# Performance work log

Measured on AMD Instinct MI355X. Metric: run time of the kernel, lower is better.

The kernel has to match this reference:

```python
import jax, jax.numpy as jnp
import numpy as np

B, S, V, E, H = 2048, 128, 128, 300, 512  # batch, max_length, vocab, embed, hidden (enc_outstate_dim == H)


def setup_inputs() -> dict:
    key = jax.random.key(0)
    ks = jax.random.split(key, 20)
    s = 0.05
    return {
        "x": jax.random.randint(ks[0], (B, 1), 0, V),
        "hidden": jax.random.normal(ks[1], (1, B, H), jnp.float32),
        "enc_output": jax.random.normal(ks[2], (B, S, H), jnp.float32),
        "emb_table": jax.random.normal(ks[3], (V, E), jnp.float32) * s,
        "W1_w": jax.random.normal(ks[4], (H, H), jnp.float32) * s,
        "W1_b": jnp.zeros((H,), jnp.float32),
        "W2_w": jax.random.normal(ks[5], (H, H), jnp.float32) * s,
        "W2_b": jnp.zeros((H,), jnp.float32),
        "V_w": jax.random.normal(ks[6], (1, H), jnp.float32) * s,
        "V_b": jnp.zeros((1,), jnp.float32),
        "gru_w_ih": jax.random.normal(ks[7], (3 * H, E + H), jnp.float32) * s,
        "gru_w_hh": jax.random.normal(ks[8], (3 * H, H), jnp.float32) * s,
        "gru_b_ih": jnp.zeros((3 * H,), jnp.float32),
        "gru_b_hh": jnp.zeros((3 * H,), jnp.float32),
        "fc1_w": jax.random.normal(ks[9], (E, H), jnp.float32) * s,
        "fc1_b": jnp.zeros((E,), jnp.float32),
        "fc2_w": jax.random.normal(ks[10], (V, E), jnp.float32) * s,
        "fc2_b": jnp.zeros((V,), jnp.float32),
    }


def reference(x, hidden, enc_output, emb_table, W1_w, W1_b, W2_w, W2_b, V_w, V_b,
              gru_w_ih, gru_w_hh, gru_b_ih, gru_b_hh, fc1_w, fc1_b, fc2_w, fc2_b):
    emb = emb_table[x[:, 0]]  # [B,E]
    # Bahdanau additive attention
    hsum = jnp.sum(hidden, axis=0)  # [B,H] (sum over layers)
    score = jnp.tanh(enc_output @ W1_w.T + W1_b + (hsum @ W2_w.T + W2_b)[:, None, :])  # [B,S,H]
    attw = jax.nn.softmax(score @ V_w.T + V_b, axis=1)  # [B,S,1]
    ctx = jnp.sum(attw * enc_output, axis=1)  # [B,H]
    # single-step GRU (PyTorch gate layout: r,z,n)
    gin = jnp.concatenate([ctx, emb], axis=-1)  # [B,H+E]
    h0 = hidden[0]
    gi = gin @ gru_w_ih.T + gru_b_ih
    gh = h0 @ gru_w_hh.T + gru_b_hh
    i_r, i_z, i_n = gi[:, :H], gi[:, H:2 * H], gi[:, 2 * H:]
    h_r, h_z, h_n = gh[:, :H], gh[:, H:2 * H], gh[:, 2 * H:]
    r = jax.nn.sigmoid(i_r + h_r)
    z = jax.nn.sigmoid(i_z + h_z)
    n = jnp.tanh(i_n + r * h_n)
    h_new = (1.0 - z) * n + z * h0  # [B,H]
    # FC head
    y = jax.nn.leaky_relu(h_new @ fc1_w.T + fc1_b, 0.01) @ fc2_w.T + fc2_b  # [B,V]
    return y, h_new[None]
```

## Files before the change

kernel.cpp:

```cpp
#include <hip/hip_runtime.h>


typedef __attribute__((ext_vector_type(4))) float floatx4;
typedef __attribute__((ext_vector_type(8))) short short8;

#define DEV static __device__ __forceinline__

DEV unsigned short f2bf(float f) {
  unsigned u = __float_as_uint(f);
  u = u + 0x7fffu + ((u >> 16) & 1u);
  return (unsigned short)(u >> 16);
}
DEV float bf2f(unsigned short s) { return __uint_as_float(((unsigned)s) << 16); }
DEV float tanh_fast(float x) {
  float e = __expf(2.f * x);
  return 1.f - 2.f / (e + 1.f);
}
DEV float sigmoid_fast(float x) { return 1.f / (1.f + __expf(-x)); }

__global__ void convpad_kernel(const float* __restrict__ src,
                               unsigned short* __restrict__ dst,
                               int Nsrc, int Kin, int Kp) {
  int idx = blockIdx.x * 256 + threadIdx.x;
  int n = idx / Kp, k = idx - n * Kp;
  float v = (k < Kin && n < Nsrc) ? src[(size_t)n * Kin + k] : 0.f;
  dst[idx] = f2bf(v);
}

__global__ void prep_bias_kernel(const float* __restrict__ W1b,
                                 const float* __restrict__ W2b,
                                 float* __restrict__ keyb,
                                 const float* __restrict__ fc1b,
                                 float* __restrict__ fc1bp) {
  int i = blockIdx.x * 256 + threadIdx.x;
  if (i < 512) keyb[i] = W1b[i] + W2b[i];
  if (i < 384) fc1bp[i] = (i < 300) ? fc1b[i] : 0.f;
}

__global__ void emb_kernel(const int* __restrict__ x,
                           const float* __restrict__ embt,
                           unsigned short* __restrict__ gin) {
  int b = blockIdx.x, e = threadIdx.x;
  float v = (e < 300) ? embt[(size_t)x[b] * 300 + e] : 0.f;
  gin[(size_t)b * 832 + 512 + e] = f2bf(v);
}

template <int EPI>
__global__ __launch_bounds__(256, 3) void gemm_bt(
    const unsigned short* __restrict__ A, int lda,
    const unsigned short* __restrict__ Bm, int ldb,
    const float* __restrict__ bias,
    void* __restrict__ Cp, int ldc, int K) {
  __shared__ unsigned short As[128 * 64];
  __shared__ unsigned short Bs[128 * 64];
  int tid = threadIdx.x;
  int bm = blockIdx.x * 128, bn = blockIdx.y * 128;
  int lane = tid & 63, wave = tid >> 6;
  int l15 = lane & 15, l4 = lane >> 4;
  int wm = (wave >> 1) * 64, wn = (wave & 1) * 64;

  floatx4 zero = {0.f, 0.f, 0.f, 0.f};
  floatx4 acc[4][4];
#pragma unroll
  for (int i = 0; i < 4; ++i)
#pragma unroll
    for (int j = 0; j < 4; ++j) acc[i][j] = zero;

  int row = tid >> 1;
  int gc0 = (tid & 1) * 4;
  const unsigned short* Aptr = A + (size_t)(bm + row) * lda + gc0 * 8;
  const unsigned short* Bptr = Bm + (size_t)(bn + row) * ldb + gc0 * 8;
  int rslot7 = row & 7, lslot7 = l15 & 7;

  int nk = K >> 6;
  for (int kt = 0; kt < nk; ++kt) {
#pragma unroll
    for (int i = 0; i < 4; ++i) {
      int slot = (gc0 + i) ^ rslot7;
      *(uint4*)&As[row * 64 + slot * 8] = *(const uint4*)(Aptr + kt * 64 + i * 8);
      *(uint4*)&Bs[row * 64 + slot * 8] = *(const uint4*)(Bptr + kt * 64 + i * 8);
    }
    __syncthreads();
#pragma unroll
    for (int ks = 0; ks < 2; ++ks) {
      int slot = (ks * 4 + l4) ^ lslot7;
      short8 av[4], bv[4];
#pragma unroll
      for (int mt = 0; mt < 4; ++mt)
        av[mt] = *(const short8*)&As[(wm + mt * 16 + l15) * 64 + slot * 8];
#pragma unroll
      for (int nt = 0; nt < 4; ++nt)
        bv[nt] = *(const short8*)&Bs[(wn + nt * 16 + l15) * 64 + slot * 8];
#pragma unroll
      for (int mt = 0; mt < 4; ++mt)
#pragma unroll
        for (int nt = 0; nt < 4; ++nt)
          acc[mt][nt] = __builtin_amdgcn_mfma_f32_16x16x32_bf16(
              av[mt], bv[nt], acc[mt][nt], 0, 0, 0);
    }
    __syncthreads();
  }

#pragma unroll
  for (int nt = 0; nt < 4; ++nt) {
    int n = bn + wn + nt * 16 + l15;
    float bvv = bias[n];
#pragma unroll
    for (int mt = 0; mt < 4; ++mt) {
#pragma unroll
      for (int r = 0; r < 4; ++r) {
        int m = bm + wm + mt * 16 + l4 * 4 + r;
        float v = acc[mt][nt][r] + bvv;
        if (EPI == 1) {
          v = v > 0.f ? v : 0.01f * v;
          ((unsigned short*)Cp)[(size_t)m * ldc + n] = f2bf(v);
        } else {
          ((float*)Cp)[(size_t)m * ldc + n] = v;
        }
      }
    }
  }
}

#define ATTN_LDS_BYTES (128 * 512 * 2 + 2 * 128 * 4)

__global__ __launch_bounds__(512, 2) void attn_kernel(
    const float* __restrict__ enc, const unsigned short* __restrict__ W1b16,
    const float* __restrict__ key, const float* __restrict__ Vw,
    unsigned short* __restrict__ gin) {
  extern __shared__ unsigned char smem_raw[];
  unsigned short* Albs = (unsigned short*)smem_raw;
  float* lds_logits = (float*)(smem_raw + 128 * 512 * 2);
  float* lds_attw = lds_logits + 128;

  int b = blockIdx.x;
  int tid = threadIdx.x;
  const float* encb = enc + (size_t)b * 128 * 512;

  if (tid < 128) lds_logits[tid] = 0.f;

#pragma unroll 2
  for (int it = 0; it < 16; ++it) {
    int g = it * 512 + tid;
    int m = g >> 6, gc = g & 63;
    const float4* src = (const float4*)(encb + (size_t)g * 8);
    float4 lo = src[0], hi = src[1];
    uint4 pk;
    pk.x = (unsigned)f2bf(lo.x) | ((unsigned)f2bf(lo.y) << 16);
    pk.y = (unsigned)f2bf(lo.z) | ((unsigned)f2bf(lo.w) << 16);
    pk.z = (unsigned)f2bf(hi.x) | ((unsigned)f2bf(hi.y) << 16);
    pk.w = (unsigned)f2bf(hi.z) | ((unsigned)f2bf(hi.w) << 16);
    int slot = gc ^ (m & 7);
    *(uint4*)&Albs[m * 512 + slot * 8] = pk;
  }
  __syncthreads();

  int wave = tid >> 6, lane = tid & 63;
  int l15 = lane & 15, l4 = lane >> 4, lslot7 = l15 & 7;
  int n0 = wave * 64;

  floatx4 zero = {0.f, 0.f, 0.f, 0.f};
  floatx4 acc[8][4];
#pragma unroll
  for (int i = 0; i < 8; ++i)
#pragma unroll
    for (int j = 0; j < 4; ++j) acc[i][j] = zero;

#pragma unroll 2
  for (int kt = 0; kt < 16; ++kt) {
    int slot = (kt * 4 + l4) ^ lslot7;
    short8 av[8], bv[4];
#pragma unroll
    for (int nt = 0; nt < 4; ++nt) {
      int n = n0 + nt * 16 + l15;
      bv[nt] = *(const short8*)(W1b16 + (size_t)n * 512 + kt * 32 + l4 * 8);
    }
#pragma unroll
    for (int mt = 0; mt < 8; ++mt)
      av[mt] = *(const short8*)&Albs[(mt * 16 + l15) * 512 + slot * 8];
#pragma unroll
    for (int mt = 0; mt < 8; ++mt)
#pragma unroll
      for (int nt = 0; nt < 4; ++nt)
        acc[mt][nt] = __builtin_amdgcn_mfma_f32_16x16x32_bf16(
            av[mt], bv[nt], acc[mt][nt], 0, 0, 0);
  }

  float kb[4], vwl[4];
#pragma unroll
  for (int nt = 0; nt < 4; ++nt) {
    int col = n0 + nt * 16 + l15;
    kb[nt] = key[(size_t)b * 512 + col];
    vwl[nt] = Vw[col];
  }
#pragma unroll
  for (int mt = 0; mt < 8; ++mt) {
#pragma unroll
    for (int r = 0; r < 4; ++r) {
      float c = 0.f;
#pragma unroll
      for (int nt = 0; nt < 4; ++nt)
        c += tanh_fast(acc[mt][nt][r] + kb[nt]) * vwl[nt];
      c += __shfl_xor(c, 1, 64);
      c += __shfl_xor(c, 2, 64);
      c += __shfl_xor(c, 4, 64);
      c += __shfl_xor(c, 8, 64);
      if (l15 == 0) atomicAdd(&lds_logits[mt * 16 + l4 * 4 + r], c);
    }
  }
  __syncthreads();

  if (wave == 0) {
    float l0 = lds_logits[lane], l1 = lds_logits[lane + 64];
    float mx = fmaxf(l0, l1);
#pragma unroll
    for (int o = 32; o >= 1; o >>= 1) mx = fmaxf(mx, __shfl_xor(mx, o, 64));
    float e0 = __expf(l0 - mx), e1 = __expf(l1 - mx);
    float s = e0 + e1;
#pragma unroll
    for (int o = 32; o >= 1; o >>= 1) s += __shfl_xor(s, o, 64);
    float inv = 1.f / s;
    lds_attw[lane] = e0 * inv;
    lds_attw[lane + 64] = e1 * inv;
  }
  __syncthreads();

  int h = tid, gc = h >> 3, off = h & 7;
  float cx = 0.f;
  for (int s = 0; s < 128; ++s)
    cx += lds_attw[s] * bf2f(Albs[s * 512 + ((gc ^ (s & 7)) << 3) + off]);
  gin[(size_t)b * 832 + h] = f2bf(cx);
}

__global__ void gru_kernel(const float* __restrict__ gi,
                           const float* __restrict__ gh,
                           const float* __restrict__ hidden,
                           float* __restrict__ outh,
                           unsigned short* __restrict__ hnewbf) {
  int idx = blockIdx.x * 256 + threadIdx.x;
  int b = idx >> 9, h = idx & 511;
  const float* gib = gi + (size_t)b * 1536;
  const float* ghb = gh + (size_t)b * 1536;
  float r = sigmoid_fast(gib[h] + ghb[h]);
  float z = sigmoid_fast(gib[512 + h] + ghb[512 + h]);
  float n = tanh_fast(gib[1024 + h] + r * ghb[1024 + h]);
  float h0 = hidden[idx];
  float hn = (1.f - z) * n + z * h0;
  outh[idx] = hn;
  hnewbf[idx] = f2bf(hn);
}

extern "C" void kernel_launch(void* const* d_in, const int* in_sizes, int n_in,
                              void* d_out, int out_size, void* d_ws,
                              size_t ws_size, hipStream_t stream) {
  const int* x = (const int*)d_in[0];
  const float* hidden = (const float*)d_in[1];
  const float* enc = (const float*)d_in[2];
  const float* embt = (const float*)d_in[3];
  const float* W1w = (const float*)d_in[4];
  const float* W1b = (const float*)d_in[5];
  const float* W2w = (const float*)d_in[6];
  const float* W2b = (const float*)d_in[7];
  const float* Vw = (const float*)d_in[8];
  const float* wih = (const float*)d_in[10];
  const float* whh = (const float*)d_in[11];
  const float* bih = (const float*)d_in[12];
  const float* bhh = (const float*)d_in[13];
  const float* fc1w = (const float*)d_in[14];
  const float* fc1b = (const float*)d_in[15];
  const float* fc2w = (const float*)d_in[16];
  const float* fc2b = (const float*)d_in[17];

  float* out_y = (float*)d_out;
  float* out_h = out_y + 2048 * 128;

  char* ws = (char*)d_ws;
  size_t o = 0;
  auto alloc = [&](size_t bytes) {
    size_t r = o;
    o += (bytes + 255) & ~(size_t)255;
    return r;
  };
  unsigned short* W1bf = (unsigned short*)(ws + alloc(512 * 512 * 2));
  unsigned short* W2bf = (unsigned short*)(ws + alloc(512 * 512 * 2));
  unsigned short* wihbf = (unsigned short*)(ws + alloc(1536 * 832 * 2));
  unsigned short* whhbf = (unsigned short*)(ws + alloc(1536 * 512 * 2));
  unsigned short* fc1wbf = (unsigned short*)(ws + alloc(384 * 512 * 2));
  unsigned short* fc2wbf = (unsigned short*)(ws + alloc(128 * 384 * 2));
  unsigned short* hidbf = (unsigned short*)(ws + alloc(2048 * 512 * 2));
  unsigned short* ginbf = (unsigned short*)(ws + alloc((size_t)2048 * 832 * 2));
  float* keyb = (float*)(ws + alloc(512 * 4));
  float* fc1bp = (float*)(ws + alloc(384 * 4));
  float* key = (float*)(ws + alloc((size_t)2048 * 512 * 4));
  float* gi = (float*)(ws + alloc((size_t)2048 * 1536 * 4));
  float* gh = (float*)(ws + alloc((size_t)2048 * 1536 * 4));
  unsigned short* hnewbf = (unsigned short*)(ws + alloc(2048 * 512 * 2));
  unsigned short* a1bf = (unsigned short*)(ws + alloc((size_t)2048 * 384 * 2));

  convpad_kernel<<<512 * 512 / 256, 256, 0, stream>>>(W1w, W1bf, 512, 512, 512);
  convpad_kernel<<<512 * 512 / 256, 256, 0, stream>>>(W2w, W2bf, 512, 512, 512);
  convpad_kernel<<<1536 * 832 / 256, 256, 0, stream>>>(wih, wihbf, 1536, 812, 832);
  convpad_kernel<<<1536 * 512 / 256, 256, 0, stream>>>(whh, whhbf, 1536, 512, 512);
  convpad_kernel<<<384 * 512 / 256, 256, 0, stream>>>(fc1w, fc1wbf, 300, 512, 512);
  convpad_kernel<<<128 * 384 / 256, 256, 0, stream>>>(fc2w, fc2wbf, 128, 300, 384);
  convpad_kernel<<<2048 * 512 / 256, 256, 0, stream>>>(hidden, hidbf, 2048, 512, 512);
  prep_bias_kernel<<<2, 256, 0, stream>>>(W1b, W2b, keyb, fc1b, fc1bp);
  emb_kernel<<<2048, 320, 0, stream>>>(x, embt, ginbf);

  gemm_bt<0><<<dim3(16, 4), 256, 0, stream>>>(hidbf, 512, W2bf, 512, keyb,
                                              (void*)key, 512, 512);

  (void)hipFuncSetAttribute((const void*)attn_kernel,
                            hipFuncAttributeMaxDynamicSharedMemorySize,
                            ATTN_LDS_BYTES);
  attn_kernel<<<2048, 512, ATTN_LDS_BYTES, stream>>>(enc, W1bf, key, Vw, ginbf);

  gemm_bt<0><<<dim3(16, 12), 256, 0, stream>>>(hidbf, 512, whhbf, 512, bhh,
                                               (void*)gh, 1536, 512);
  gemm_bt<0><<<dim3(16, 12), 256, 0, stream>>>(ginbf, 832, wihbf, 832, bih,
                                               (void*)gi, 1536, 832);
  gru_kernel<<<2048 * 512 / 256, 256, 0, stream>>>(gi, gh, hidden, out_h, hnewbf);

  gemm_bt<1><<<dim3(16, 3), 256, 0, stream>>>(hnewbf, 512, fc1wbf, 512, fc1bp,
                                              (void*)a1bf, 384, 512);
  gemm_bt<0><<<dim3(16, 1), 256, 0, stream>>>(a1bf, 384, fc2wbf, 384, fc2b,
                                              (void*)out_y, 128, 384);
}
```

Baseline: 1.019 ms.

## Fuse prep kernels, merge key/gh GEMMs, pipeline attention enc load and GEMM tiles

```diff
diff --git a/kernel.cpp b/kernel.cpp
--- a/kernel.cpp
+++ b/kernel.cpp
@@ -3,56 +3,92 @@
 
 typedef __attribute__((ext_vector_type(4))) float floatx4;
 typedef __attribute__((ext_vector_type(8))) short short8;
+typedef unsigned short us;
 
 #define DEV static __device__ __forceinline__
 
-DEV unsigned short f2bf(float f) {
+DEV us f2bf(float f) {
   unsigned u = __float_as_uint(f);
   u = u + 0x7fffu + ((u >> 16) & 1u);
-  return (unsigned short)(u >> 16);
-}
-DEV float bf2f(unsigned short s) { return __uint_as_float(((unsigned)s) << 16); }
+  return (us)(u >> 16);
+}
+DEV float bf2f(us s) { return __uint_as_float(((unsigned)s) << 16); }
 DEV float tanh_fast(float x) {
   float e = __expf(2.f * x);
   return 1.f - 2.f / (e + 1.f);
 }
 DEV float sigmoid_fast(float x) { return 1.f / (1.f + __expf(-x)); }
-
-__global__ void convpad_kernel(const float* __restrict__ src,
-                               unsigned short* __restrict__ dst,
-                               int Nsrc, int Kin, int Kp) {
+DEV unsigned pack2(float a, float b) {
+  return (unsigned)f2bf(a) | ((unsigned)f2bf(b) << 16);
+}
+
+#define S0 262144
+#define S1 1310720
+#define S2 2588672
+#define S3 2785280
+#define S4 2834432
+#define S5 3883008
+#define S6 3885056
+#define S7 3885440
+#define S8 4540800
+
+__global__ void prep_kernel(const float* __restrict__ W1w,
+                            const float* __restrict__ W2w,
+                            const float* __restrict__ whh,
+                            const float* __restrict__ wih,
+                            const float* __restrict__ fc1w,
+                            const float* __restrict__ fc2w,
+                            const float* __restrict__ hidden,
+                            const float* __restrict__ W1b,
+                            const float* __restrict__ W2b,
+                            const float* __restrict__ bhh,
+                            const float* __restrict__ fc1b,
+                            const int* __restrict__ x,
+                            const float* __restrict__ embt,
+                            us* __restrict__ W1bf, us* __restrict__ wcomb,
+                            us* __restrict__ wihbf, us* __restrict__ fc1wbf,
+                            us* __restrict__ fc2wbf, us* __restrict__ hidbf,
+                            float* __restrict__ bcomb,
+                            float* __restrict__ fc1bp,
+                            us* __restrict__ ginbf) {
   int idx = blockIdx.x * 256 + threadIdx.x;
-  int n = idx / Kp, k = idx - n * Kp;
-  float v = (k < Kin && n < Nsrc) ? src[(size_t)n * Kin + k] : 0.f;
-  dst[idx] = f2bf(v);
-}
-
-__global__ void prep_bias_kernel(const float* __restrict__ W1b,
-                                 const float* __restrict__ W2b,
-                                 float* __restrict__ keyb,
-                                 const float* __restrict__ fc1b,
-                                 float* __restrict__ fc1bp) {
-  int i = blockIdx.x * 256 + threadIdx.x;
-  if (i < 512) keyb[i] = W1b[i] + W2b[i];
-  if (i < 384) fc1bp[i] = (i < 300) ? fc1b[i] : 0.f;
-}
-
-__global__ void emb_kernel(const int* __restrict__ x,
-                           const float* __restrict__ embt,
-                           unsigned short* __restrict__ gin) {
-  int b = blockIdx.x, e = threadIdx.x;
-  float v = (e < 300) ? embt[(size_t)x[b] * 300 + e] : 0.f;
-  gin[(size_t)b * 832 + 512 + e] = f2bf(v);
+  if (idx < S0) {
+    W1bf[idx] = f2bf(W1w[idx]);
+  } else if (idx < S1) {
+    int i = idx - S0, n = i >> 9, k = i & 511;
+    float v = (n < 512) ? W2w[i] : whh[(size_t)(n - 512) * 512 + k];
+    wcomb[i] = f2bf(v);
+  } else if (idx < S2) {
+    int i = idx - S1, n = i / 832, k = i - n * 832;
+    wihbf[i] = f2bf(k < 812 ? wih[(size_t)n * 812 + k] : 0.f);
+  } else if (idx < S3) {
+    int i = idx - S2, n = i >> 9;
+    fc1wbf[i] = f2bf(n < 300 ? fc1w[i] : 0.f);
+  } else if (idx < S4) {
+    int i = idx - S3, n = i / 384, k = i - n * 384;
+    fc2wbf[i] = f2bf(k < 300 ? fc2w[(size_t)n * 300 + k] : 0.f);
+  } else if (idx < S5) {
+    int i = idx - S4;
+    hidbf[i] = f2bf(hidden[i]);
+  } else if (idx < S6) {
+    int i = idx - S5;
+    bcomb[i] = (i < 512) ? (W1b[i] + W2b[i]) : bhh[i - 512];
+  } else if (idx < S7) {
+    int i = idx - S6;
+    fc1bp[i] = (i < 300) ? fc1b[i] : 0.f;
+  } else if (idx < S8) {
+    int i = idx - S7, b = i / 320, e = i - b * 320;
+    float v = (e < 300) ? embt[(size_t)x[b] * 300 + e] : 0.f;
+    ginbf[(size_t)b * 832 + 512 + e] = f2bf(v);
+  }
 }
 
 template <int EPI>
 __global__ __launch_bounds__(256, 3) void gemm_bt(
-    const unsigned short* __restrict__ A, int lda,
-    const unsigned short* __restrict__ Bm, int ldb,
-    const float* __restrict__ bias,
-    void* __restrict__ Cp, int ldc, int K) {
-  __shared__ unsigned short As[128 * 64];
-  __shared__ unsigned short Bs[128 * 64];
+    const us* __restrict__ A, int lda, const us* __restrict__ Bm, int ldb,
+    const float* __restrict__ bias, void* __restrict__ Cp, int ldc, int K) {
+  __shared__ us As[128 * 64];
+  __shared__ us Bs[128 * 64];
   int tid = threadIdx.x;
   int bm = blockIdx.x * 128, bn = blockIdx.y * 128;
   int lane = tid & 63, wave = tid >> 6;
@@ -68,19 +104,34 @@
 
   int row = tid >> 1;
   int gc0 = (tid & 1) * 4;
-  const unsigned short* Aptr = A + (size_t)(bm + row) * lda + gc0 * 8;
-  const unsigned short* Bptr = Bm + (size_t)(bn + row) * ldb + gc0 * 8;
+  const us* Aptr = A + (size_t)(bm + row) * lda + gc0 * 8;
+  const us* Bptr = Bm + (size_t)(bn + row) * ldb + gc0 * 8;
   int rslot7 = row & 7, lslot7 = l15 & 7;
+
+  uint4 pa[4], pb[4];
+#pragma unroll
+  for (int i = 0; i < 4; ++i) {
+    pa[i] = *(const uint4*)(Aptr + i * 8);
+    pb[i] = *(const uint4*)(Bptr + i * 8);
+  }
 
   int nk = K >> 6;
   for (int kt = 0; kt < nk; ++kt) {
+    if (kt) __syncthreads();
 #pragma unroll
     for (int i = 0; i < 4; ++i) {
       int slot = (gc0 + i) ^ rslot7;
-      *(uint4*)&As[row * 64 + slot * 8] = *(const uint4*)(Aptr + kt * 64 + i * 8);
-      *(uint4*)&Bs[row * 64 + slot * 8] = *(const uint4*)(Bptr + kt * 64 + i * 8);
+      *(uint4*)&As[row * 64 + slot * 8] = pa[i];
+      *(uint4*)&Bs[row * 64 + slot * 8] = pb[i];
     }
     __syncthreads();
+    if (kt + 1 < nk) {
+#pragma unroll
+      for (int i = 0; i < 4; ++i) {
+        pa[i] = *(const uint4*)(Aptr + (kt + 1) * 64 + i * 8);
+        pb[i] = *(const uint4*)(Bptr + (kt + 1) * 64 + i * 8);
+      }
+    }
 #pragma unroll
     for (int ks = 0; ks < 2; ++ks) {
       int slot = (ks * 4 + l4) ^ lslot7;
@@ -98,7 +149,6 @@
           acc[mt][nt] = __builtin_amdgcn_mfma_f32_16x16x32_bf16(
               av[mt], bv[nt], acc[mt][nt], 0, 0, 0);
     }
-    __syncthreads();
   }
 
 #pragma unroll
@@ -113,7 +163,7 @@
         float v = acc[mt][nt][r] + bvv;
         if (EPI == 1) {
           v = v > 0.f ? v : 0.01f * v;
-          ((unsigned short*)Cp)[(size_t)m * ldc + n] = f2bf(v);
+          ((us*)Cp)[(size_t)m * ldc + n] = f2bf(v);
         } else {
           ((float*)Cp)[(size_t)m * ldc + n] = v;
         }
@@ -122,43 +172,32 @@
   }
 }
 
-#define ATTN_LDS_BYTES (128 * 512 * 2 + 2 * 128 * 4)
+#define ATTN_LDS_BYTES (131072 + 512 + 512 + 2048)
 
 __global__ __launch_bounds__(512, 2) void attn_kernel(
-    const float* __restrict__ enc, const unsigned short* __restrict__ W1b16,
-    const float* __restrict__ key, const float* __restrict__ Vw,
-    unsigned short* __restrict__ gin) {
-  extern __shared__ unsigned char smem_raw[];
-  unsigned short* Albs = (unsigned short*)smem_raw;
-  float* lds_logits = (float*)(smem_raw + 128 * 512 * 2);
+    const float* __restrict__ enc, const us* __restrict__ W1b16,
+    const float* __restrict__ keygh, const float* __restrict__ Vw,
+    us* __restrict__ gin) {
+  extern __shared__ unsigned char smem[];
+  us* Albs = (us*)smem;
+  float* lds_logits = (float*)(smem + 131072);
   float* lds_attw = lds_logits + 128;
-
-  int b = blockIdx.x;
-  int tid = threadIdx.x;
-  const float* encb = enc + (size_t)b * 128 * 512;
-
+  float* lds_ctx = lds_attw + 128;
+
+  int b = blockIdx.x, tid = threadIdx.x;
+  const float* encb = enc + (size_t)b * 65536;
   if (tid < 128) lds_logits[tid] = 0.f;
-
-#pragma unroll 2
-  for (int it = 0; it < 16; ++it) {
-    int g = it * 512 + tid;
-    int m = g >> 6, gc = g & 63;
-    const float4* src = (const float4*)(encb + (size_t)g * 8);
-    float4 lo = src[0], hi = src[1];
-    uint4 pk;
-    pk.x = (unsigned)f2bf(lo.x) | ((unsigned)f2bf(lo.y) << 16);
-    pk.y = (unsigned)f2bf(lo.z) | ((unsigned)f2bf(lo.w) << 16);
-    pk.z = (unsigned)f2bf(hi.x) | ((unsigned)f2bf(hi.y) << 16);
-    pk.w = (unsigned)f2bf(hi.z) | ((unsigned)f2bf(hi.w) << 16);
-    int slot = gc ^ (m & 7);
-    *(uint4*)&Albs[m * 512 + slot * 8] = pk;
-  }
-  __syncthreads();
 
   int wave = tid >> 6, lane = tid & 63;
   int l15 = lane & 15, l4 = lane >> 4, lslot7 = l15 & 7;
   int n0 = wave * 64;
 
+  int srow = tid >> 2, g0 = tid & 3;
+  int c7 = srow & 7;
+  int slotA = g0 ^ c7, slotB = (g0 + 4) ^ c7;
+  const float* sp = encb + srow * 512 + g0 * 8;
+  us* wbase = Albs + srow * 64;
+
   floatx4 zero = {0.f, 0.f, 0.f, 0.f};
   floatx4 acc[8][4];
 #pragma unroll
@@ -166,31 +205,57 @@
 #pragma unroll
     for (int j = 0; j < 4; ++j) acc[i][j] = zero;
 
-#pragma unroll 2
-  for (int kt = 0; kt < 16; ++kt) {
-    int slot = (kt * 4 + l4) ^ lslot7;
-    short8 av[8], bv[4];
-#pragma unroll
-    for (int nt = 0; nt < 4; ++nt) {
-      int n = n0 + nt * 16 + l15;
-      bv[nt] = *(const short8*)(W1b16 + (size_t)n * 512 + kt * 32 + l4 * 8);
-    }
-#pragma unroll
-    for (int mt = 0; mt < 8; ++mt)
-      av[mt] = *(const short8*)&Albs[(mt * 16 + l15) * 512 + slot * 8];
-#pragma unroll
-    for (int mt = 0; mt < 8; ++mt)
-#pragma unroll
-      for (int nt = 0; nt < 4; ++nt)
-        acc[mt][nt] = __builtin_amdgcn_mfma_f32_16x16x32_bf16(
-            av[mt], bv[nt], acc[mt][nt], 0, 0, 0);
+  float4 p0, p1, p2, p3;
+  p0 = *(const float4*)(sp + 0);
+  p1 = *(const float4*)(sp + 4);
+  p2 = *(const float4*)(sp + 32);
+  p3 = *(const float4*)(sp + 36);
+
+  for (int kt = 0; kt < 8; ++kt) {
+    uint4 qa, qb;
+    qa.x = pack2(p0.x, p0.y); qa.y = pack2(p0.z, p0.w);
+    qa.z = pack2(p1.x, p1.y); qa.w = pack2(p1.z, p1.w);
+    qb.x = pack2(p2.x, p2.y); qb.y = pack2(p2.z, p2.w);
+    qb.z = pack2(p3.x, p3.y); qb.w = pack2(p3.z, p3.w);
+    us* wb = wbase + kt * 8192;
+    *(uint4*)(wb + slotA * 8) = qa;
+    *(uint4*)(wb + slotB * 8) = qb;
+    __syncthreads();
+    if (kt < 7) {
+      const float* np = sp + (kt + 1) * 64;
+      p0 = *(const float4*)(np + 0);
+      p1 = *(const float4*)(np + 4);
+      p2 = *(const float4*)(np + 32);
+      p3 = *(const float4*)(np + 36);
+    }
+#pragma unroll
+    for (int ks = 0; ks < 2; ++ks) {
+      short8 av[8], bv[4];
+#pragma unroll
+      for (int nt = 0; nt < 4; ++nt) {
+        int n = n0 + nt * 16 + l15;
+        bv[nt] = *(const short8*)(W1b16 + (size_t)n * 512 + kt * 64 +
+                                  ks * 32 + l4 * 8);
+      }
+      int slot = (ks * 4 + l4) ^ lslot7;
+      const us* rb = Albs + kt * 8192;
+#pragma unroll
+      for (int mt = 0; mt < 8; ++mt)
+        av[mt] = *(const short8*)(rb + (mt * 16 + l15) * 64 + slot * 8);
+#pragma unroll
+      for (int mt = 0; mt < 8; ++mt)
+#pragma unroll
+        for (int nt = 0; nt < 4; ++nt)
+          acc[mt][nt] = __builtin_amdgcn_mfma_f32_16x16x32_bf16(
+              av[mt], bv[nt], acc[mt][nt], 0, 0, 0);
+    }
   }
 
   float kb[4], vwl[4];
 #pragma unroll
   for (int nt = 0; nt < 4; ++nt) {
     int col = n0 + nt * 16 + l15;
-    kb[nt] = key[(size_t)b * 512 + col];
+    kb[nt] = keygh[(size_t)b * 2048 + col];
     vwl[nt] = Vw[col];
   }
 #pragma unroll
@@ -211,11 +276,11 @@
   __syncthreads();
 
   if (wave == 0) {
-    float l0 = lds_logits[lane], l1 = lds_logits[lane + 64];
-    float mx = fmaxf(l0, l1);
+    float v0 = lds_logits[lane], v1 = lds_logits[lane + 64];
+    float mx = fmaxf(v0, v1);
 #pragma unroll
     for (int o = 32; o >= 1; o >>= 1) mx = fmaxf(mx, __shfl_xor(mx, o, 64));
-    float e0 = __expf(l0 - mx), e1 = __expf(l1 - mx);
+    float e0 = __expf(v0 - mx), e1 = __expf(v1 - mx);
     float s = e0 + e1;
 #pragma unroll
     for (int o = 32; o >= 1; o >>= 1) s += __shfl_xor(s, o, 64);
@@ -225,22 +290,36 @@
   }
   __syncthreads();
 
-  int h = tid, gc = h >> 3, off = h & 7;
-  float cx = 0.f;
-  for (int s = 0; s < 128; ++s)
-    cx += lds_attw[s] * bf2f(Albs[s * 512 + ((gc ^ (s & 7)) << 3) + off]);
-  gin[(size_t)b * 832 + h] = f2bf(cx);
+  int pr = tid & 255, sh = tid >> 8;
+  int h0 = pr * 2;
+  int ktc = h0 >> 6, gclc = (h0 & 63) >> 3, dofs = (pr & 3) * 2;
+  const us* cb = Albs + ktc * 8192;
+  float c0 = 0.f, c1 = 0.f;
+  int sbeg = sh * 64;
+  for (int s = sbeg; s < sbeg + 64; ++s) {
+    int slot = gclc ^ (s & 7);
+    unsigned d = *(const unsigned*)(cb + s * 64 + slot * 8 + dofs);
+    float aw = lds_attw[s];
+    c0 += aw * bf2f((us)(d & 0xffffu));
+    c1 += aw * bf2f((us)(d >> 16));
+  }
+  if (sh == 0) { lds_ctx[h0] = c0; lds_ctx[h0 + 1] = c1; }
+  __syncthreads();
+  if (sh == 1) {
+    unsigned pk = pack2(lds_ctx[h0] + c0, lds_ctx[h0 + 1] + c1);
+    *(unsigned*)(gin + (size_t)b * 832 + h0) = pk;
+  }
 }
 
 __global__ void gru_kernel(const float* __restrict__ gi,
-                           const float* __restrict__ gh,
+                           const float* __restrict__ keygh,
                            const float* __restrict__ hidden,
                            float* __restrict__ outh,
-                           unsigned short* __restrict__ hnewbf) {
+                           us* __restrict__ hnewbf) {
   int idx = blockIdx.x * 256 + threadIdx.x;
   int b = idx >> 9, h = idx & 511;
   const float* gib = gi + (size_t)b * 1536;
-  const float* ghb = gh + (size_t)b * 1536;
+  const float* ghb = keygh + (size_t)b * 2048 + 512;
   float r = sigmoid_fast(gib[h] + ghb[h]);
   float z = sigmoid_fast(gib[512 + h] + ghb[512 + h]);
   float n = tanh_fast(gib[1024 + h] + r * ghb[1024 + h]);
@@ -281,45 +360,38 @@
     o += (bytes + 255) & ~(size_t)255;
     return r;
   };
-  unsigned short* W1bf = (unsigned short*)(ws + alloc(512 * 512 * 2));
-  unsigned short* W2bf = (unsigned short*)(ws + alloc(512 * 512 * 2));
-  unsigned short* wihbf = (unsigned short*)(ws + alloc(1536 * 832 * 2));
-  unsigned short* whhbf = (unsigned short*)(ws + alloc(1536 * 512 * 2));
-  unsigned short* fc1wbf = (unsigned short*)(ws + alloc(384 * 512 * 2));
-  unsigned short* fc2wbf = (unsigned short*)(ws + alloc(128 * 384 * 2));
-  unsigned short* hidbf = (unsigned short*)(ws + alloc(2048 * 512 * 2));
-  unsigned short* ginbf = (unsigned short*)(ws + alloc((size_t)2048 * 832 * 2));
-  float* keyb = (float*)(ws + alloc(512 * 4));
+  us* W1bf   = (us*)(ws + alloc(512 * 512 * 2));
+  us* wcomb  = (us*)(ws + alloc(2048 * 512 * 2));
+  us* wihbf  = (us*)(ws + alloc(1536 * 832 * 2));
+  us* fc1wbf = (us*)(ws + alloc(384 * 512 * 2));
+  us* fc2wbf = (us*)(ws + alloc(128 * 384 * 2));
+  us* hidbf  = (us*)(ws + alloc(2048 * 512 * 2));
+  float* bcomb = (float*)(ws + alloc(2048 * 4));
   float* fc1bp = (float*)(ws + alloc(384 * 4));
-  float* key = (float*)(ws + alloc((size_t)2048 * 512 * 4));
-  float* gi = (float*)(ws + alloc((size_t)2048 * 1536 * 4));
-  float* gh = (float*)(ws + alloc((size_t)2048 * 1536 * 4));
-  unsigned short* hnewbf = (unsigned short*)(ws + alloc(2048 * 512 * 2));
-  unsigned short* a1bf = (unsigned short*)(ws + alloc((size_t)2048 * 384 * 2));
-
-  convpad_kernel<<<512 * 512 / 256, 256, 0, stream>>>(W1w, W1bf, 512, 512, 512);
-  convpad_kernel<<<512 * 512 / 256, 256, 0, stream>>>(W2w, W2bf, 512, 512, 512);
-  convpad_kernel<<<1536 * 832 / 256, 256, 0, stream>>>(wih, wihbf, 1536, 812, 832);
-  convpad_kernel<<<1536 * 512 / 256, 256, 0, stream>>>(whh, whhbf, 1536, 512, 512);
-  convpad_kernel<<<384 * 512 / 256, 256, 0, stream>>>(fc1w, fc1wbf, 300, 512, 512);
-  convpad_kernel<<<128 * 384 / 256, 256, 0, stream>>>(fc2w, fc2wbf, 128, 300, 384);
-  convpad_kernel<<<2048 * 512 / 256, 256, 0, stream>>>(hidden, hidbf, 2048, 512, 512);
-  prep_bias_kernel<<<2, 256, 0, stream>>>(W1b, W2b, keyb, fc1b, fc1bp);
-  emb_kernel<<<2048, 320, 0, stream>>>(x, embt, ginbf);
-
-  gemm_bt<0><<<dim3(16, 4), 256, 0, stream>>>(hidbf, 512, W2bf, 512, keyb,
-                                              (void*)key, 512, 512);
+  us* ginbf  = (us*)(ws + alloc((size_t)2048 * 832 * 2));
+  float* keygh = (float*)(ws + alloc((size_t)2048 * 2048 * 4));
+  float* gi    = (float*)(ws + alloc((size_t)2048 * 1536 * 4));
+  us* hnewbf = (us*)(ws + alloc(2048 * 512 * 2));
+  us* a1bf   = (us*)(ws + alloc((size_t)2048 * 384 * 2));
+
+  prep_kernel<<<(S8 + 255) / 256, 256, 0, stream>>>(
+      W1w, W2w, whh, wih, fc1w, fc2w, hidden, W1b, W2b, bhh, fc1b, x, embt,
+      W1bf, wcomb, wihbf, fc1wbf, fc2wbf, hidbf, bcomb, fc1bp, ginbf);
+
+  gemm_bt<0><<<dim3(16, 16), 256, 0, stream>>>(hidbf, 512, wcomb, 512, bcomb,
+                                               (void*)keygh, 2048, 512);
 
   (void)hipFuncSetAttribute((const void*)attn_kernel,
                             hipFuncAttributeMaxDynamicSharedMemorySize,
                             ATTN_LDS_BYTES);
-  attn_kernel<<<2048, 512, ATTN_LDS_BYTES, stream>>>(enc, W1bf, key, Vw, ginbf);
-
-  gemm_bt<0><<<dim3(16, 12), 256, 0, stream>>>(hidbf, 512, whhbf, 512, bhh,
-                                               (void*)gh, 1536, 512);
+  attn_kernel<<<2048, 512, ATTN_LDS_BYTES, stream>>>(enc, W1bf, keygh, Vw,
+                                                     ginbf);
+
   gemm_bt<0><<<dim3(16, 12), 256, 0, stream>>>(ginbf, 832, wihbf, 832, bih,
                                                (void*)gi, 1536, 832);
-  gru_kernel<<<2048 * 512 / 256, 256, 0, stream>>>(gi, gh, hidden, out_h, hnewbf);
+
+  gru_kernel<<<2048 * 512 / 256, 256, 0, stream>>>(gi, keygh, hidden, out_h,
+                                                   hnewbf);
 
   gemm_bt<1><<<dim3(16, 3), 256, 0, stream>>>(hnewbf, 512, fc1wbf, 512, fc1bp,
                                               (void*)a1bf, 384, 512);
```

After: 1.039 ms. About the same (+2.0%).
